# Performance work log

Measured on AMD Instinct MI355X. Metric: run time of the kernel, lower is better.

The kernel has to match this reference:

```python
import jax, jax.numpy as jnp
import numpy as np

H = 4  # num_heads


def _ln(x, g, b, eps=1e-5):
    m = x.mean(-1, keepdims=True)
    v = ((x - m) ** 2).mean(-1, keepdims=True)
    return (x - m) / jnp.sqrt(v + eps) * g + b


def setup_inputs() -> dict:
    key = jax.random.key(0)
    ks = jax.random.split(key, 16)
    B, N, M, dQ, dK, dV = 4, 2048, 2048, 128, 128, 128
    s = 0.02
    return {
        "Q": jax.random.normal(ks[0], (B, N, dQ), jnp.float32),
        "K": jax.random.normal(ks[1], (B, M, dK), jnp.float32),
        "adj_mask": jax.random.randint(ks[2], (B, N, M), 0, 2, jnp.int32),
        "Wq": jax.random.normal(ks[3], (dQ, dV), jnp.float32) * s,
        "bq": jnp.zeros((dV,), jnp.float32),
        "Wk": jax.random.normal(ks[4], (dK, dV), jnp.float32) * s,
        "bk": jnp.zeros((dV,), jnp.float32),
        "Wv": jax.random.normal(ks[5], (dK, dV), jnp.float32) * s,
        "bv": jnp.zeros((dV,), jnp.float32),
        "Wr1": jax.random.normal(ks[6], (dV, dV), jnp.float32) * s,
        "br1": jnp.zeros((dV,), jnp.float32),
        "Wr2": jax.random.normal(ks[7], (dV, dV), jnp.float32) * s,
        "br2": jnp.zeros((dV,), jnp.float32),
        "g0": jnp.ones((dV,), jnp.float32),
        "be0": jnp.zeros((dV,), jnp.float32),
        "g1": jnp.ones((dV,), jnp.float32),
        "be1": jnp.zeros((dV,), jnp.float32),
    }


def reference(Q, K, adj_mask, Wq, bq, Wk, bk, Wv, bv, Wr1, br1, Wr2, br2, g0, be0, g1, be1):
    B, N, _ = Q.shape
    M = K.shape[1]
    dV = Wq.shape[1]
    dh = dV // H
    Qp = Q @ Wq + bq   # [B,N,dV]
    Kp = K @ Wk + bk   # [B,M,dV]
    Vp = K @ Wv + bv   # [B,M,dV]
    # torch: split dim_V into H chunks, cat along dim 0 -> head-major [H*B, L, dh]
    def to_heads(x, L):
        return x.reshape(B, L, H, dh).transpose(2, 0, 1, 3).reshape(H * B, L, dh)
    Qh, Kh, Vh = to_heads(Qp, N), to_heads(Kp, M), to_heads(Vp, M)
    attn = jnp.einsum('bnd,bmd->bnm', Qh, Kh) / jnp.sqrt(jnp.float32(dh))  # [H*B,N,M]
    # torch repeat_interleave(mask, H, dim=0) gives batch-major order -- faithful
    mask = jnp.repeat(adj_mask, H, axis=0)
    attn = jnp.where(mask == 0, -jnp.inf, attn)
    A = jax.nn.softmax(attn, axis=2)
    O = Qh + jnp.einsum('bnm,bmd->bnd', A, Vh)  # [H*B,N,dh]
    # recombine heads back to [B,N,dV] (intended split(dim=0)/cat(dim=2))
    O = O.reshape(H, B, N, dh).transpose(1, 2, 0, 3).reshape(B, N, dV)
    O = _ln(O, g0, be0)
    O = O + (jax.nn.relu(O @ Wr1 + br1) @ Wr2 + br2)
    return _ln(O, g1, be1)
```

## Files before the change

### kernel.cpp

```cpp
#include <hip/hip_runtime.h>
#include <hip/hip_bf16.h>


typedef short bf16x8 __attribute__((ext_vector_type(8)));
typedef float f32x4 __attribute__((ext_vector_type(4)));

#define BN 4
#define SEQ 2048
#define DIM 128
#define NH 4
#define DH 32
#define ROWS (BN * SEQ)
#define MS 4
#define MWORDS (SEQ / 32)

static __device__ __forceinline__ unsigned short f2bf(float f) {
    __hip_bfloat16 h = __float2bfloat16(f);
    return *reinterpret_cast<unsigned short*>(&h);
}
static __device__ __forceinline__ float bf2f(unsigned short u) {
    union { unsigned int i; float f; } cv;
    cv.i = ((unsigned int)u) << 16;
    return cv.f;
}
static __device__ __forceinline__ unsigned int pack2bf(float a, float b) {
    return (unsigned int)f2bf(a) | ((unsigned int)f2bf(b) << 16);
}

__global__ __launch_bounds__(256) void pack_prep(
    const int* __restrict__ adj,
    const float* __restrict__ Wq, const float* __restrict__ Wk,
    const float* __restrict__ Wv, const float* __restrict__ W1,
    const float* __restrict__ W2,
    unsigned int* __restrict__ bits, unsigned short* __restrict__ WT)
{
    const int bx = blockIdx.x;
    if (bx >= 2048) {
        const float* Ws[5] = {Wq, Wk, Wv, W1, W2};
        const float* W = Ws[bx - 2048];
        unsigned short* out = WT + (bx - 2048) * DIM * DIM;
        for (int i = threadIdx.x; i < DIM * DIM; i += 256) {
            int n = i >> 7, k = i & 127;
            out[i] = f2bf(W[k * DIM + n]);
        }
        return;
    }
    const int wid = bx * 256 + threadIdx.x;
    const int4* src = (const int4*)(adj + (long)wid * 32);
    unsigned int w = 0;
#pragma unroll
    for (int j = 0; j < 8; ++j) {
        int4 v = src[j];
        w |= (((unsigned)v.x & 1u) << (4 * j))
           | (((unsigned)v.y & 1u) << (4 * j + 1))
           | (((unsigned)v.z & 1u) << (4 * j + 2))
           | (((unsigned)v.w & 1u) << (4 * j + 3));
    }
    const int q = wid >> 6;
    const int wd = wid & 63;
    bits[((long)(q >> 11) * MWORDS + wd) * SEQ + (q & 2047)] = w;
}

__global__ __launch_bounds__(256) void proj_kernel(
    const float* __restrict__ Q, const float* __restrict__ K,
    const float* __restrict__ bq, const float* __restrict__ bk,
    const float* __restrict__ bv, const unsigned short* __restrict__ WT,
    float* __restrict__ Qp, unsigned short* __restrict__ Qb,
    unsigned short* __restrict__ Kb, unsigned short* __restrict__ Vt)
{
    __shared__ __align__(16) unsigned short sX[32][136];
    __shared__ __align__(16) unsigned short sY[32][137];

    const int proj = blockIdx.y;
    const int rowbase = blockIdx.x * 32;
    const float* X = (proj == 0) ? Q : K;
    const unsigned short* Wt = WT + proj * DIM * DIM;
    const float* bias = (proj == 0) ? bq : (proj == 1) ? bk : bv;
    const int bidx = rowbase >> 11;
    const int srowbase = rowbase & 2047;

    const int t = threadIdx.x;
#pragma unroll
    for (int i = 0; i < 4; ++i) {
        int idx = i * 256 + t;
        int row = idx >> 5, c4 = (idx & 31) * 4;
        float4 v = *(const float4*)(X + (long)(rowbase + row) * DIM + c4);
        sX[row][c4 + 0] = f2bf(v.x);
        sX[row][c4 + 1] = f2bf(v.y);
        sX[row][c4 + 2] = f2bf(v.z);
        sX[row][c4 + 3] = f2bf(v.w);
    }
    __syncthreads();

    const int w = t >> 6, lane = t & 63;
    const int n16 = lane & 15, quad = lane >> 4;

    f32x4 acc[2][2];
#pragma unroll
    for (int r = 0; r < 2; ++r)
#pragma unroll
        for (int ct = 0; ct < 2; ++ct)
            acc[r][ct] = (f32x4){0.f, 0.f, 0.f, 0.f};

    for (int ks = 0; ks < 4; ++ks) {
        bf16x8 bfrag[2];
#pragma unroll
        for (int ct = 0; ct < 2; ++ct) {
            int ncol = w * 32 + ct * 16 + n16;
            bfrag[ct] = *(const bf16x8*)(Wt + ncol * DIM + ks * 32 + quad * 8);
        }
#pragma unroll
        for (int r = 0; r < 2; ++r) {
            bf16x8 afrag = *(const bf16x8*)(&sX[r * 16 + n16][ks * 32 + quad * 8]);
#pragma unroll
            for (int ct = 0; ct < 2; ++ct)
                acc[r][ct] = __builtin_amdgcn_mfma_f32_16x16x32_bf16(
                    afrag, bfrag[ct], acc[r][ct], 0, 0, 0);
        }
    }

#pragma unroll
    for (int r = 0; r < 2; ++r) {
#pragma unroll
        for (int ct = 0; ct < 2; ++ct) {
            int col = w * 32 + ct * 16 + n16;
            int hh = col >> 5, dd = col & 31;
            float bv_ = bias[col];
#pragma unroll
            for (int i = 0; i < 4; ++i) {
                int lrow = r * 16 + quad * 4 + i;
                int grow = rowbase + lrow;
                int srow = srowbase + lrow;
                float val = acc[r][ct][i] + bv_;
                if (proj == 0) {
                    Qp[(long)grow * DIM + col] = val;
                    Qb[((long)(hh * BN + bidx) * SEQ + srow) * DH + dd]
                        = f2bf(val * 0.17677669529663687f);
                } else if (proj == 1) {
                    Kb[((long)(hh * BN + bidx) * SEQ + srow) * DH + dd] = f2bf(val);
                } else {
                    sY[lrow][col] = f2bf(val);
                }
            }
        }
    }
    if (proj == 2) {
        __syncthreads();
#pragma unroll
        for (int i = 0; i < 16; ++i) {
            int idx = i * 256 + t;
            int c = idx >> 5, m = idx & 31;
            Vt[((long)bidx * DIM + c) * SEQ + srowbase + m] = sY[m][c];
        }
    }
}

__global__ __launch_bounds__(256, 4) void attn_kernel(
    const unsigned short* __restrict__ Qb, const unsigned short* __restrict__ Kb,
    const unsigned short* __restrict__ Vt, const unsigned int* __restrict__ mbits,
    unsigned short* __restrict__ Opart, float* __restrict__ Lpart)
{
    __shared__ __align__(16) unsigned short sP[4][32][68];

    const int h = blockIdx.y;
    const int qbase = blockIdx.x * 32;
    const int sp = blockIdx.z;
    const int t = threadIdx.x;
    const int b = t >> 6;
    const int lane = t & 63, n16 = lane & 15, quad = lane >> 4;

    const unsigned short* Qh = Qb + ((long)(h * BN + b) * SEQ) * DH + quad * 8;
    const unsigned short* Kp = Kb + ((long)(h * BN + b) * SEQ) * DH + quad * 8;
    const unsigned short* Vp = Vt + ((long)b * DIM + h * DH) * SEQ + quad * 8;
    const unsigned int*   Mp = mbits + ((long)h * MWORDS + sp * 16) * SEQ + qbase + n16;

    bf16x8 qfrag[2];
#pragma unroll
    for (int r = 0; r < 2; ++r)
        qfrag[r] = *(const bf16x8*)(Qh + (long)(qbase + r * 16 + n16) * DH);

    f32x4 o[2][2];
    float lsum[2];
#pragma unroll
    for (int r = 0; r < 2; ++r) {
#pragma unroll
        for (int ct = 0; ct < 2; ++ct) o[r][ct] = (f32x4){0.f, 0.f, 0.f, 0.f};
        lsum[r] = 0.f;
    }

    bf16x8 kf[2][2], vf[2][2];
    unsigned int mw[2][2];
    const int mb0 = sp * 512;

#pragma unroll
    for (int c = 0; c < 2; ++c) {
        kf[0][c] = *(const bf16x8*)(Kp + (long)(mb0 + c * 16 + n16) * DH);
        vf[0][c] = *(const bf16x8*)(Vp + (long)(c * 16 + n16) * SEQ + mb0);
    }
#pragma unroll
    for (int r = 0; r < 2; ++r) mw[0][r] = Mp[r * 16];

    const f32x4 zero4 = {0.f, 0.f, 0.f, 0.f};

#pragma unroll
    for (int mt = 0; mt < 16; ++mt) {
        const int cur = mt & 1, nxt = cur ^ 1;
        if (mt < 15) {
            const int mb = mb0 + (mt + 1) * 32;
#pragma unroll
            for (int c = 0; c < 2; ++c) {
                kf[nxt][c] = *(const bf16x8*)(Kp + (long)(mb + c * 16 + n16) * DH);
                vf[nxt][c] = *(const bf16x8*)(Vp + (long)(c * 16 + n16) * SEQ + mb);
            }
#pragma unroll
            for (int r = 0; r < 2; ++r) mw[nxt][r] = Mp[(long)(mt + 1) * SEQ + r * 16];
        }
#pragma unroll
        for (int r = 0; r < 2; ++r) {
            f32x4 st[2];
#pragma unroll
            for (int c = 0; c < 2; ++c)
                st[c] = __builtin_amdgcn_mfma_f32_16x16x32_bf16(
                    kf[cur][c], qfrag[r], zero4, 0, 0, 0);
            const unsigned int wm = mw[cur][r];
            float p[2][4];
#pragma unroll
            for (int c = 0; c < 2; ++c)
#pragma unroll
                for (int i = 0; i < 4; ++i) {
                    float e = __expf(st[c][i]);
                    p[c][i] = ((wm >> (c * 16 + quad * 4 + i)) & 1u) ? e : 0.f;
                    lsum[r] += p[c][i];
                }
#pragma unroll
            for (int c = 0; c < 2; ++c) {
                uint2 wv;
                wv.x = pack2bf(p[c][0], p[c][1]);
                wv.y = pack2bf(p[c][2], p[c][3]);
                *(uint2*)&sP[b][r * 16 + n16][c * 16 + quad * 4] = wv;
            }
        }
#pragma unroll
        for (int r = 0; r < 2; ++r) {
            bf16x8 pa = *(const bf16x8*)(&sP[b][r * 16 + n16][quad * 8]);
#pragma unroll
            for (int ct = 0; ct < 2; ++ct)
                o[r][ct] = __builtin_amdgcn_mfma_f32_16x16x32_bf16(
                    pa, vf[cur][ct], o[r][ct], 0, 0, 0);
        }
    }

#pragma unroll
    for (int r = 0; r < 2; ++r) {
        lsum[r] += __shfl_xor(lsum[r], 16, 64);
        lsum[r] += __shfl_xor(lsum[r], 32, 64);
    }

    unsigned short* Ob = Opart + ((long)sp * ROWS + (long)b * SEQ) * DIM;
#pragma unroll
    for (int r = 0; r < 2; ++r)
#pragma unroll
        for (int ct = 0; ct < 2; ++ct)
#pragma unroll
            for (int i = 0; i < 4; ++i)
                Ob[(long)(qbase + r * 16 + quad * 4 + i) * DIM + h * DH + ct * 16 + n16]
                    = f2bf(o[r][ct][i]);

    if (quad == 0) {
#pragma unroll
        for (int r = 0; r < 2; ++r)
            Lpart[(((long)sp * BN + b) * NH + h) * SEQ + qbase + r * 16 + n16] = lsum[r];
    }
}

__global__ __launch_bounds__(256) void epi_kernel(
    const float* __restrict__ Qp, const unsigned short* __restrict__ Opart,
    const float* __restrict__ Lpart, const unsigned short* __restrict__ WT,
    const float* __restrict__ br1, const float* __restrict__ br2,
    const float* __restrict__ g0, const float* __restrict__ be0,
    const float* __restrict__ g1, const float* __restrict__ be1,
    float* __restrict__ out)
{
    __shared__ __align__(16) unsigned short sXb[16][136];
    __shared__ __align__(16) unsigned short sHb[16][136];
    __shared__ __align__(16) float sXf[16][132];

    const int rowbase = blockIdx.x * 16;
    const int t = threadIdx.x;
    const int row = t >> 4, col8 = (t & 15) * 8;
    const int grow = rowbase + row;
    const int bidx = grow >> 11;
    const int srow = grow & 2047;
    const int head = col8 >> 5;

    {
        float l = 0.f;
#pragma unroll
        for (int s = 0; s < MS; ++s)
            l += Lpart[(((long)s * BN + bidx) * NH + head) * SEQ + srow];
        float linv = 1.f / l;

        float ovf[8];
#pragma unroll
        for (int j = 0; j < 8; ++j) ovf[j] = 0.f;
#pragma unroll
        for (int s = 0; s < MS; ++s) {
            bf16x8 p = *(const bf16x8*)(Opart + ((long)s * ROWS + grow) * DIM + col8);
#pragma unroll
            for (int j = 0; j < 8; ++j) ovf[j] += bf2f((unsigned short)p[j]);
        }

        float vals[8];
        float sum = 0.f, ss = 0.f;
#pragma unroll
        for (int j = 0; j < 8; j += 4) {
            float4 qv = *(const float4*)(Qp + (long)grow * DIM + col8 + j);
            vals[j + 0] = qv.x + ovf[j + 0] * linv;
            vals[j + 1] = qv.y + ovf[j + 1] * linv;
            vals[j + 2] = qv.z + ovf[j + 2] * linv;
            vals[j + 3] = qv.w + ovf[j + 3] * linv;
#pragma unroll
            for (int u = 0; u < 4; ++u) { sum += vals[j + u]; ss += vals[j + u] * vals[j + u]; }
        }
        sum += __shfl_xor(sum, 1, 64); sum += __shfl_xor(sum, 2, 64);
        sum += __shfl_xor(sum, 4, 64); sum += __shfl_xor(sum, 8, 64);
        ss  += __shfl_xor(ss, 1, 64);  ss  += __shfl_xor(ss, 2, 64);
        ss  += __shfl_xor(ss, 4, 64);  ss  += __shfl_xor(ss, 8, 64);
        float mean = sum * (1.f / 128.f);
        float var  = ss * (1.f / 128.f) - mean * mean;
        float rstd = rsqrtf(var + 1e-5f);
#pragma unroll
        for (int j = 0; j < 8; ++j) {
            int col = col8 + j;
            float x = (vals[j] - mean) * rstd * g0[col] + be0[col];
            sXf[row][col] = x;
            sXb[row][col] = f2bf(x);
        }
    }
    __syncthreads();

    const int w = t >> 6, lane = t & 63;
    const int n16 = lane & 15, quad = lane >> 4;
    const unsigned short* W1t = WT + 3 * DIM * DIM;
    const unsigned short* W2t = WT + 4 * DIM * DIM;

    f32x4 acc[2];
#pragma unroll
    for (int ct = 0; ct < 2; ++ct) acc[ct] = (f32x4){0.f, 0.f, 0.f, 0.f};
    for (int ks = 0; ks < 4; ++ks) {
        bf16x8 afrag = *(const bf16x8*)(&sXb[n16][ks * 32 + quad * 8]);
#pragma unroll
        for (int ct = 0; ct < 2; ++ct) {
            bf16x8 bfrag = *(const bf16x8*)(W1t + (w * 32 + ct * 16 + n16) * DIM + ks * 32 + quad * 8);
            acc[ct] = __builtin_amdgcn_mfma_f32_16x16x32_bf16(afrag, bfrag, acc[ct], 0, 0, 0);
        }
    }
#pragma unroll
    for (int ct = 0; ct < 2; ++ct) {
        int col = w * 32 + ct * 16 + n16;
        float bb = br1[col];
#pragma unroll
        for (int i = 0; i < 4; ++i) {
            float hv = acc[ct][i] + bb;
            sHb[quad * 4 + i][col] = f2bf(fmaxf(hv, 0.f));
        }
    }
    __syncthreads();

    f32x4 acc2[2];
#pragma unroll
    for (int ct = 0; ct < 2; ++ct) acc2[ct] = (f32x4){0.f, 0.f, 0.f, 0.f};
    for (int ks = 0; ks < 4; ++ks) {
        bf16x8 afrag = *(const bf16x8*)(&sHb[n16][ks * 32 + quad * 8]);
#pragma unroll
        for (int ct = 0; ct < 2; ++ct) {
            bf16x8 bfrag = *(const bf16x8*)(W2t + (w * 32 + ct * 16 + n16) * DIM + ks * 32 + quad * 8);
            acc2[ct] = __builtin_amdgcn_mfma_f32_16x16x32_bf16(afrag, bfrag, acc2[ct], 0, 0, 0);
        }
    }
    float yv[2][4];
#pragma unroll
    for (int ct = 0; ct < 2; ++ct) {
        int col = w * 32 + ct * 16 + n16;
        float bb = br2[col];
#pragma unroll
        for (int i = 0; i < 4; ++i)
            yv[ct][i] = acc2[ct][i] + bb + sXf[quad * 4 + i][col];
    }
    __syncthreads();
#pragma unroll
    for (int ct = 0; ct < 2; ++ct) {
        int col = w * 32 + ct * 16 + n16;
#pragma unroll
        for (int i = 0; i < 4; ++i)
            sXf[quad * 4 + i][col] = yv[ct][i];
    }
    __syncthreads();

    {
        float vals[8];
        float sum = 0.f, ss = 0.f;
#pragma unroll
        for (int j = 0; j < 8; ++j) {
            float v = sXf[row][col8 + j];
            vals[j] = v; sum += v; ss += v * v;
        }
        sum += __shfl_xor(sum, 1, 64); sum += __shfl_xor(sum, 2, 64);
        sum += __shfl_xor(sum, 4, 64); sum += __shfl_xor(sum, 8, 64);
        ss  += __shfl_xor(ss, 1, 64);  ss  += __shfl_xor(ss, 2, 64);
        ss  += __shfl_xor(ss, 4, 64);  ss  += __shfl_xor(ss, 8, 64);
        float mean = sum * (1.f / 128.f);
        float var  = ss * (1.f / 128.f) - mean * mean;
        float rstd = rsqrtf(var + 1e-5f);
        float* op = out + (long)grow * DIM + col8;
#pragma unroll
        for (int j = 0; j < 8; j += 4) {
            float4 ov;
            int col = col8 + j;
            ov.x = (vals[j + 0] - mean) * rstd * g1[col + 0] + be1[col + 0];
            ov.y = (vals[j + 1] - mean) * rstd * g1[col + 1] + be1[col + 1];
            ov.z = (vals[j + 2] - mean) * rstd * g1[col + 2] + be1[col + 2];
            ov.w = (vals[j + 3] - mean) * rstd * g1[col + 3] + be1[col + 3];
            *(float4*)(op + j) = ov;
        }
    }
}

extern "C" void kernel_launch(void* const* d_in, const int* in_sizes, int n_in,
                              void* d_out, int out_size, void* d_ws, size_t ws_size,
                              hipStream_t stream) {
    const float* Q   = (const float*)d_in[0];
    const float* K   = (const float*)d_in[1];
    const int*   adj = (const int*)d_in[2];
    const float* Wq  = (const float*)d_in[3];
    const float* bq  = (const float*)d_in[4];
    const float* Wk  = (const float*)d_in[5];
    const float* bk  = (const float*)d_in[6];
    const float* Wv  = (const float*)d_in[7];
    const float* bv  = (const float*)d_in[8];
    const float* Wr1 = (const float*)d_in[9];
    const float* br1 = (const float*)d_in[10];
    const float* Wr2 = (const float*)d_in[11];
    const float* br2 = (const float*)d_in[12];
    const float* g0  = (const float*)d_in[13];
    const float* be0 = (const float*)d_in[14];
    const float* g1  = (const float*)d_in[15];
    const float* be1 = (const float*)d_in[16];
    float* out = (float*)d_out;

    float* Qp             = (float*)d_ws;
    unsigned short* Opart = (unsigned short*)(Qp + (long)ROWS * DIM);
    float* Lpart          = (float*)(Opart + (long)MS * ROWS * DIM);
    unsigned short* Qb    = (unsigned short*)(Lpart + (long)MS * BN * NH * SEQ);
    unsigned short* Kb    = Qb + (long)ROWS * DIM;
    unsigned short* Vt    = Kb + (long)ROWS * DIM;
    unsigned short* WT    = Vt + (long)ROWS * DIM;
    unsigned int*   bits  = (unsigned int*)(WT + 5 * DIM * DIM);

    pack_prep<<<2053, 256, 0, stream>>>(adj, Wq, Wk, Wv, Wr1, Wr2, bits, WT);
    proj_kernel<<<dim3(256, 3), 256, 0, stream>>>(Q, K, bq, bk, bv, WT,
                                                  Qp, Qb, Kb, Vt);
    attn_kernel<<<dim3(64, NH, MS), 256, 0, stream>>>(Qb, Kb, Vt, bits, Opart, Lpart);
    epi_kernel<<<512, 256, 0, stream>>>(Qp, Opart, Lpart, WT, br1, br2,
                                        g0, be0, g1, be1, out);
}
```

Before: 205.0 us.

## Coalesce mask bit transposes, attention partial stores, and remap attention grid

The mask packer now has each block handle 32 query rows. It stages the packed words in shared memory and writes the transposed bit layout with coalesced stores, instead of one scattered 4-byte store per thread. The attention kernel stages its output tile in shared memory and writes contiguous 1KB chunks into a new head-major Opart layout, and the epilogue reads that layout. The attention grid is flattened so that the head and split blocks for the same query tile are adjacent, which may improve mask and Q reuse in cache. This adds shared memory traffic and a barrier in exchange for fewer strided global writes.

```diff
diff --git a/kernel.cpp b/kernel.cpp
--- a/kernel.cpp
+++ b/kernel.cpp
@@ -35,30 +35,43 @@
     unsigned int* __restrict__ bits, unsigned short* __restrict__ WT)
 {
     const int bx = blockIdx.x;
-    if (bx >= 2048) {
+    const int t = threadIdx.x;
+    if (bx >= 256) {
         const float* Ws[5] = {Wq, Wk, Wv, W1, W2};
-        const float* W = Ws[bx - 2048];
-        unsigned short* out = WT + (bx - 2048) * DIM * DIM;
-        for (int i = threadIdx.x; i < DIM * DIM; i += 256) {
+        const float* W = Ws[bx - 256];
+        unsigned short* out = WT + (bx - 256) * DIM * DIM;
+        for (int i = t; i < DIM * DIM; i += 256) {
             int n = i >> 7, k = i & 127;
             out[i] = f2bf(W[k * DIM + n]);
         }
         return;
     }
-    const int wid = bx * 256 + threadIdx.x;
-    const int4* src = (const int4*)(adj + (long)wid * 32);
-    unsigned int w = 0;
-#pragma unroll
-    for (int j = 0; j < 8; ++j) {
-        int4 v = src[j];
-        w |= (((unsigned)v.x & 1u) << (4 * j))
-           | (((unsigned)v.y & 1u) << (4 * j + 1))
-           | (((unsigned)v.z & 1u) << (4 * j + 2))
-           | (((unsigned)v.w & 1u) << (4 * j + 3));
-    }
-    const int q = wid >> 6;
-    const int wd = wid & 63;
-    bits[((long)(q >> 11) * MWORDS + wd) * SEQ + (q & 2047)] = w;
+    __shared__ unsigned int sB[32][65];
+    const int q0 = bx * 32;
+#pragma unroll
+    for (int i = 0; i < 8; ++i) {
+        int widl = i * 256 + t;
+        int ql = widl >> 6, wd = widl & 63;
+        const int4* src = (const int4*)(adj + (long)(q0 + ql) * SEQ + wd * 32);
+        unsigned int w = 0;
+#pragma unroll
+        for (int j = 0; j < 8; ++j) {
+            int4 v = src[j];
+            w |= (((unsigned)v.x & 1u) << (4 * j))
+               | (((unsigned)v.y & 1u) << (4 * j + 1))
+               | (((unsigned)v.z & 1u) << (4 * j + 2))
+               | (((unsigned)v.w & 1u) << (4 * j + 3));
+        }
+        sB[ql][wd] = w;
+    }
+    __syncthreads();
+    const int h = q0 >> 11, qh0 = q0 & 2047;
+#pragma unroll
+    for (int i = 0; i < 8; ++i) {
+        int idx = i * 256 + t;
+        int wd = idx >> 5, ql = idx & 31;
+        bits[((long)h * MWORDS + wd) * SEQ + qh0 + ql] = sB[ql][wd];
+    }
 }
 
 __global__ __launch_bounds__(256) void proj_kernel(
@@ -162,9 +175,12 @@
 {
     __shared__ __align__(16) unsigned short sP[4][32][68];
 
-    const int h = blockIdx.y;
-    const int qbase = blockIdx.x * 32;
-    const int sp = blockIdx.z;
+    const int id = blockIdx.x;
+    const int combo = id & 15;
+    const int qidx = id >> 4;
+    const int h = combo >> 2;
+    const int sp = combo & 3;
+    const int qbase = qidx * 32;
     const int t = threadIdx.x;
     const int b = t >> 6;
     const int lane = t & 63, n16 = lane & 15, quad = lane >> 4;
@@ -256,15 +272,21 @@
         lsum[r] += __shfl_xor(lsum[r], 32, 64);
     }
 
-    unsigned short* Ob = Opart + ((long)sp * ROWS + (long)b * SEQ) * DIM;
 #pragma unroll
     for (int r = 0; r < 2; ++r)
 #pragma unroll
         for (int ct = 0; ct < 2; ++ct)
 #pragma unroll
             for (int i = 0; i < 4; ++i)
-                Ob[(long)(qbase + r * 16 + quad * 4 + i) * DIM + h * DH + ct * 16 + n16]
-                    = f2bf(o[r][ct][i]);
+                sP[b][r * 16 + quad * 4 + i][ct * 16 + n16] = f2bf(o[r][ct][i]);
+    {
+        const uint4 w0 = *(const uint4*)&sP[b][lane >> 1][(lane & 1) * 16];
+        const uint4 w1 = *(const uint4*)&sP[b][lane >> 1][(lane & 1) * 16 + 8];
+        unsigned short* Ob = Opart
+            + ((((long)sp * NH + h) * BN + b) * SEQ + qbase) * 32;
+        *(uint4*)(Ob + (long)lane * 16)     = w0;
+        *(uint4*)(Ob + (long)lane * 16 + 8) = w1;
+    }
 
     if (quad == 0) {
 #pragma unroll
@@ -292,6 +314,7 @@
     const int bidx = grow >> 11;
     const int srow = grow & 2047;
     const int head = col8 >> 5;
+    const int dd = col8 & 31;
 
     {
         float l = 0.f;
@@ -305,7 +328,8 @@
         for (int j = 0; j < 8; ++j) ovf[j] = 0.f;
 #pragma unroll
         for (int s = 0; s < MS; ++s) {
-            bf16x8 p = *(const bf16x8*)(Opart + ((long)s * ROWS + grow) * DIM + col8);
+            bf16x8 p = *(const bf16x8*)(Opart
+                + ((((long)s * NH + head) * BN + bidx) * SEQ + srow) * 32 + dd);
 #pragma unroll
             for (int j = 0; j < 8; ++j) ovf[j] += bf2f((unsigned short)p[j]);
         }
@@ -457,10 +481,10 @@
     unsigned short* WT    = Vt + (long)ROWS * DIM;
     unsigned int*   bits  = (unsigned int*)(WT + 5 * DIM * DIM);
 
-    pack_prep<<<2053, 256, 0, stream>>>(adj, Wq, Wk, Wv, Wr1, Wr2, bits, WT);
+    pack_prep<<<261, 256, 0, stream>>>(adj, Wq, Wk, Wv, Wr1, Wr2, bits, WT);
     proj_kernel<<<dim3(256, 3), 256, 0, stream>>>(Q, K, bq, bk, bv, WT,
                                                   Qp, Qb, Kb, Vt);
-    attn_kernel<<<dim3(64, NH, MS), 256, 0, stream>>>(Qb, Kb, Vt, bits, Opart, Lpart);
+    attn_kernel<<<1024, 256, 0, stream>>>(Qb, Kb, Vt, bits, Opart, Lpart);
     epi_kernel<<<512, 256, 0, stream>>>(Qp, Opart, Lpart, WT, br1, br2,
                                         g0, be0, g1, be1, out);
 }
```

New measurement: 207.2 us. About the same (+1.1%).
